# Performance work log

Measured on AMD Instinct MI355X. Metric: run time of the kernel, lower is better.

The kernel has to match this reference:

```python
import jax, jax.numpy as jnp
import numpy as np

B, T, D, VQ, L2, HID = 8, 2048, 768, 64, 12, 1024
K = 2 ** L2          # 4096 codebook entries
N_MID = 4            # condition_layer=6 -> 1 input + 4 middle + 1 output Linear, 5 BatchNorms
EPS_N = 1e-6
EPS_BN = 1e-5


def setup_inputs() -> dict:
    key = jax.random.key(0)
    ks = jax.random.split(key, 10)
    g = lambda i, shape, sc: jax.random.normal(ks[i], shape, jnp.float32) * sc
    return {
        "h_in": jax.random.normal(ks[0], (B, D, T), jnp.float32),
        "attn_mask": jax.random.randint(ks[1], (B, T), 0, 2, jnp.int32),
        "proj_w": g(2, (VQ, D), 0.02), "proj_b": jnp.zeros((VQ,), jnp.float32),
        "inv_w": g(3, (D, VQ), 0.02), "inv_b": jnp.zeros((D,), jnp.float32),
        "mlp_w_in": g(4, (HID, L2), 0.1), "mlp_b_in": jnp.zeros((HID,), jnp.float32),
        "mlp_w_mid": g(5, (N_MID, HID, HID), 0.03), "mlp_b_mid": jnp.zeros((N_MID, HID), jnp.float32),
        "mlp_w_out": g(6, (VQ, HID), 0.03), "mlp_b_out": jnp.zeros((VQ,), jnp.float32),
        "bn_gamma": jnp.ones((N_MID + 1, HID), jnp.float32),
        "bn_beta": jnp.zeros((N_MID + 1, HID), jnp.float32),
    }


def _bn(x, gamma, beta):
    # BatchNorm1d, training mode: batch mean / biased var over codebook rows
    m = x.mean(axis=0)
    v = x.var(axis=0)
    return (x - m) * jax.lax.rsqrt(v + EPS_BN) * gamma + beta


def _l2norm(x):
    return x / (jnp.linalg.norm(x, axis=-1, keepdims=True) + EPS_N)


def reference(h_in, attn_mask, proj_w, proj_b, inv_w, inv_b,
              mlp_w_in, mlp_b_in, mlp_w_mid, mlp_b_mid, mlp_w_out, mlp_b_out,
              bn_gamma, bn_beta):
    # --- codebook: binary vectors -> condition MLP (Linear+BN+ReLU x5, Linear) ---
    ints = jnp.arange(K)
    bits = ((ints[:, None] & (1 << jnp.arange(L2 - 1, -1, -1))) > 0).astype(jnp.float32)  # [K, L2]
    x = jax.nn.relu(_bn(bits @ mlp_w_in.T + mlp_b_in, bn_gamma[0], bn_beta[0]))
    for i in range(N_MID):
        x = jax.nn.relu(_bn(x @ mlp_w_mid[i].T + mlp_b_mid[i], bn_gamma[i + 1], bn_beta[i + 1]))
    embed = x @ mlp_w_out.T + mlp_b_out          # [K, VQ]
    embed = _l2norm(embed)                        # sphere=True

    # --- project hidden states: h_in [B,D,T] -> [B,T,VQ] ---
    h = jnp.einsum('bdt,vd->btv', h_in, proj_w) + proj_b
    h = _l2norm(h)

    # --- pairwise squared distances to codebook, argmax of -d (== softmax argmax) ---
    hf = h.reshape(-1, VQ)                                       # [B*T, VQ]
    d = (hf ** 2).sum(-1, keepdims=True) + (embed ** 2).sum(-1) - 2.0 * (hf @ embed.T)  # [B*T, K]
    code = jnp.argmax(-d, axis=-1)                               # [B*T]

    # --- masked gather/scatter quantization (eval path: hard codes) ---
    mask = (attn_mask == 1)                                      # [B, T]
    h_vq = embed[code].reshape(B, T, VQ) * mask[..., None].astype(h.dtype)
    quantized = jnp.einsum('btv,dv->btd', h_vq, inv_w) + inv_b   # proj_inv -> [B, T, D]
    vq_code = jnp.where(mask, code.reshape(B, T), 0)
    return quantized, vq_code
```

## Files before the change

kernel.cpp:

```cpp
#include <hip/hip_runtime.h>
#include <stddef.h>

#define BB   8
#define TT_  2048
#define DD   768
#define VQ_  64
#define L2C  12
#define HID_ 1024
#define KK   4096
#define NMID 4
#define NT   (BB*TT_)

typedef _Float16 h8v __attribute__((ext_vector_type(8)));
typedef float    f4v __attribute__((ext_vector_type(4)));

#define GL16(g, l) __builtin_amdgcn_global_load_lds( \
    (const __attribute__((address_space(1))) void*)(g), \
    (__attribute__((address_space(3))) void*)(l), 16, 0, 0)

__global__ __launch_bounds__(256) void k_mlp_in(const float* __restrict__ w_in,
                                                const float* __restrict__ b_in,
                                                float* __restrict__ X) {
    __shared__ float ws_[256 * 12];
    __shared__ float bs_[256];
    int tid = threadIdx.x;
    int h0  = blockIdx.x * 256;
    for (int i = tid; i < 256 * 12; i += 256) ws_[i] = w_in[h0 * 12 + i];
    bs_[tid] = b_in[h0 + tid];
    __syncthreads();
    float w[12];
#pragma unroll
    for (int l = 0; l < 12; l++) w[l] = ws_[tid * 12 + l];
    float bias = bs_[tid];
    int k0 = blockIdx.y * 16;
    for (int kk = 0; kk < 16; kk++) {
        int k = k0 + kk;
        float acc = bias;
#pragma unroll
        for (int l = 0; l < 12; l++)
            if ((k >> (11 - l)) & 1) acc += w[l];
        X[(size_t)k * HID_ + h0 + tid] = acc;
    }
}

__global__ __launch_bounds__(256) void k_bn_stats1(const float* __restrict__ Y,
                                                   float* __restrict__ part) {
    int b = blockIdx.x;
    int c = blockIdx.y * 256 + threadIdx.x;
    const float* src = Y + ((size_t)b << 6) * HID_ + c;
    float s = 0.f, q = 0.f;
    for (int r = 0; r < 64; r++) {
        float v = src[(size_t)r << 10];
        s += v; q += v * v;
    }
    part[((size_t)b << 10) + c] = s;
    part[65536 + ((size_t)b << 10) + c] = q;
}

__global__ __launch_bounds__(256) void k_bn_stats2(const float* __restrict__ part,
                                                   float* __restrict__ mv) {
    int c = blockIdx.x * 256 + threadIdx.x;
    float s = 0.f, q = 0.f;
    for (int b = 0; b < 64; b++) {
        s += part[((size_t)b << 10) + c];
        q += part[65536 + ((size_t)b << 10) + c];
    }
    float m = s * (1.f / KK);
    float v = q * (1.f / KK) - m * m;
    mv[c] = m; mv[HID_ + c] = v;
}

__global__ __launch_bounds__(256) void k_bn_apply_split(const float* __restrict__ Y,
                                                        const float* __restrict__ mv,
                                                        const float* __restrict__ gamma,
                                                        const float* __restrict__ beta,
                                                        _Float16* __restrict__ Xhi,
                                                        _Float16* __restrict__ Xlo) {
    int i = blockIdx.x * 256 + threadIdx.x;
    int c = (i << 2) & (HID_ - 1);
    float4 x = ((const float4*)Y)[i];
    float4 m = *(const float4*)(mv + c);
    float4 v = *(const float4*)(mv + HID_ + c);
    float4 g = *(const float4*)(gamma + c);
    float4 b = *(const float4*)(beta + c);
    float o[4];
    o[0] = fmaxf(0.f, (x.x - m.x) * (1.f / sqrtf(v.x + 1e-5f)) * g.x + b.x);
    o[1] = fmaxf(0.f, (x.y - m.y) * (1.f / sqrtf(v.y + 1e-5f)) * g.y + b.y);
    o[2] = fmaxf(0.f, (x.z - m.z) * (1.f / sqrtf(v.z + 1e-5f)) * g.z + b.z);
    o[3] = fmaxf(0.f, (x.w - m.w) * (1.f / sqrtf(v.w + 1e-5f)) * g.w + b.w);
    union { _Float16 h[4]; uint2 u; } uh, ul;
#pragma unroll
    for (int j = 0; j < 4; j++) {
        _Float16 h = (_Float16)o[j];
        uh.h[j] = h;
        ul.h[j] = (_Float16)(o[j] - (float)h);
    }
    *(uint2*)(Xhi + ((size_t)i << 2)) = uh.u;
    *(uint2*)(Xlo + ((size_t)i << 2)) = ul.u;
}

__global__ __launch_bounds__(256) void k_gemm_mfma3(const _Float16* __restrict__ Ahi,
                                                    const _Float16* __restrict__ Alo,
                                                    const _Float16* __restrict__ Whi,
                                                    const _Float16* __restrict__ Wlo,
                                                    const float* __restrict__ bias,
                                                    float* __restrict__ C) {
    __shared__ __attribute__((aligned(128))) char lds[4 * 32768];
    const int tid = threadIdx.x;
    const int wg = blockIdx.x;
    const int m0 = (wg & 31) << 7;
    const int n0 = (wg >> 5) << 7;
    const int wave = tid >> 6, lane = tid & 63;
    const int l15 = lane & 15, quad = lane >> 4;
    const int wm = (wave >> 1) << 6;
    const int wn = (wave & 1) << 6;

    const int rowA = (wave << 5) + (lane >> 2);
    const int colb = (lane & 3) << 4;
    const char* gA_h = (const char*)Ahi + ((size_t)(m0 + rowA) << 11) + colb;
    const char* gA_l = (const char*)Alo + ((size_t)(m0 + rowA) << 11) + colb;
    const char* gW_h = (const char*)Whi + ((size_t)(n0 + rowA) << 11) + colb;
    const char* gW_l = (const char*)Wlo + ((size_t)(n0 + rowA) << 11) + colb;
    const int dA = wave << 11;

    int offA[4], offW[4];
#pragma unroll
    for (int i = 0; i < 4; i++) offA[i] = ((wm + (i << 4) + l15) << 6) + (quad << 4);
#pragma unroll
    for (int j = 0; j < 4; j++) offW[j] = ((wn + (j << 4) + l15) << 6) + (quad << 4);

    f4v acc[4][4];
#pragma unroll
    for (int i = 0; i < 4; i++)
#pragma unroll
        for (int j = 0; j < 4; j++) acc[i][j] = (f4v){0.f, 0.f, 0.f, 0.f};

#define STG(bufi, tt) do { \
        char* b_ = lds + ((bufi) << 15); int o_ = (tt) << 6; \
        GL16(gA_h + o_,         b_ + dA); \
        GL16(gA_h + 32768 + o_, b_ + dA + 1024); \
        GL16(gA_l + o_,         b_ + 8192 + dA); \
        GL16(gA_l + 32768 + o_, b_ + 8192 + dA + 1024); \
        GL16(gW_h + o_,         b_ + 16384 + dA); \
        GL16(gW_h + 32768 + o_, b_ + 16384 + dA + 1024); \
        GL16(gW_l + o_,         b_ + 24576 + dA); \
        GL16(gW_l + 32768 + o_, b_ + 24576 + dA + 1024); \
    } while (0)

    STG(0, 0); STG(1, 1); STG(2, 2);
    for (int t = 0; t < 32; ++t) {
        if (t <= 29)      asm volatile("s_waitcnt vmcnt(16)" ::: "memory");
        else if (t == 30) asm volatile("s_waitcnt vmcnt(8)"  ::: "memory");
        else              asm volatile("s_waitcnt vmcnt(0)"  ::: "memory");
        __builtin_amdgcn_s_barrier();
        asm volatile("" ::: "memory");
        if (t + 3 < 32) STG((t + 3) & 3, t + 3);
        const char* b = lds + ((size_t)(t & 3) << 15);
        h8v ah[4], al[4];
#pragma unroll
        for (int i = 0; i < 4; i++) {
            ah[i] = *(const h8v*)(b + offA[i]);
            al[i] = *(const h8v*)(b + 8192 + offA[i]);
        }
        __builtin_amdgcn_s_setprio(1);
#pragma unroll
        for (int j = 0; j < 4; j++) {
            h8v bh = *(const h8v*)(b + 16384 + offW[j]);
            h8v bl = *(const h8v*)(b + 24576 + offW[j]);
#pragma unroll
            for (int i = 0; i < 4; i++) {
                acc[i][j] = __builtin_amdgcn_mfma_f32_16x16x32_f16(ah[i], bh, acc[i][j], 0, 0, 0);
                acc[i][j] = __builtin_amdgcn_mfma_f32_16x16x32_f16(ah[i], bl, acc[i][j], 0, 0, 0);
                acc[i][j] = __builtin_amdgcn_mfma_f32_16x16x32_f16(al[i], bh, acc[i][j], 0, 0, 0);
            }
        }
        __builtin_amdgcn_s_setprio(0);
        asm volatile("" ::: "memory");
    }
#undef STG

#pragma unroll
    for (int j = 0; j < 4; j++) {
        int col = n0 + wn + (j << 4) + l15;
        float bv = bias[col];
#pragma unroll
        for (int i = 0; i < 4; i++) {
            int row = m0 + wm + (i << 4) + (quad << 2);
#pragma unroll
            for (int r = 0; r < 4; r++)
                C[(size_t)(row + r) * HID_ + col] = acc[i][j][r] + bv;
        }
    }
}

__global__ __launch_bounds__(256) void k_gemm_mfma2(const _Float16* __restrict__ Ahi,
                                                    const _Float16* __restrict__ Alo,
                                                    const _Float16* __restrict__ Whi,
                                                    const _Float16* __restrict__ Wlo,
                                                    const float* __restrict__ bias,
                                                    float* __restrict__ C,
                                                    int M, int N, int Kd) {
    __shared__ __attribute__((aligned(128))) char lds[2][24576];
    const int tid = threadIdx.x;
    int wg = blockIdx.x;
    const int nwg = gridDim.x;
    wg = (wg & 7) * (nwg >> 3) + (wg >> 3);
    const int nx = M >> 7;
    const int m0 = (wg % nx) << 7;
    const int n0 = (wg / nx) << 6;
    const int wave = tid >> 6, lane = tid & 63;
    const int l15 = lane & 15, quad = lane >> 4;
    const int wm = (wave >> 1) << 6;
    const int wn = (wave & 1) << 5;

    const int pA0 = ((wave << 1) | 0) * 1024 + lane * 16;
    const int pA1 = ((wave << 1) | 1) * 1024 + lane * 16;
    const int pW  = wave * 1024 + lane * 16;
    const int qA0 = pA0 ^ (((pA0 >> 7) & 3) << 4);
    const int qA1 = pA1 ^ (((pA1 >> 7) & 3) << 4);
    const int qW  = pW  ^ (((pW  >> 7) & 3) << 4);
    const size_t krow = (size_t)Kd * 2;
    const char* gAh0 = (const char*)Ahi + (size_t)(m0 + (qA0 >> 6)) * krow + (qA0 & 63);
    const char* gAh1 = (const char*)Ahi + (size_t)(m0 + (qA1 >> 6)) * krow + (qA1 & 63);
    const char* gAl0 = (const char*)Alo + (size_t)(m0 + (qA0 >> 6)) * krow + (qA0 & 63);
    const char* gAl1 = (const char*)Alo + (size_t)(m0 + (qA1 >> 6)) * krow + (qA1 & 63);
    const char* gWh  = (const char*)Whi + (size_t)(n0 + (qW >> 6)) * krow + (qW & 63);
    const char* gWl  = (const char*)Wlo + (size_t)(n0 + (qW >> 6)) * krow + (qW & 63);
    const int dA0 = (wave << 1) * 1024;
    const int dA1 = dA0 + 1024;
    const int dW  = wave * 1024;

    int offA[4], offW[2];
#pragma unroll
    for (int i = 0; i < 4; i++) {
        int r = wm + (i << 4) + l15;
        offA[i] = r * 64 + ((quad ^ ((r >> 1) & 3)) << 4);
    }
#pragma unroll
    for (int j = 0; j < 2; j++) {
        int r = wn + (j << 4) + l15;
        offW[j] = r * 64 + ((quad ^ ((r >> 1) & 3)) << 4);
    }

    f4v acc[4][2];
#pragma unroll
    for (int i = 0; i < 4; i++)
#pragma unroll
        for (int j = 0; j < 2; j++) acc[i][j] = (f4v){0.f, 0.f, 0.f, 0.f};

#define STAGE(bufi, tt) do { \
        char* b_ = lds[bufi]; size_t o_ = (size_t)(tt) << 6; \
        GL16(gAh0 + o_, b_ + dA0); \
        GL16(gAh1 + o_, b_ + dA1); \
        GL16(gAl0 + o_, b_ + 8192 + dA0); \
        GL16(gAl1 + o_, b_ + 8192 + dA1); \
        GL16(gWh  + o_, b_ + 16384 + dW); \
        GL16(gWl  + o_, b_ + 20480 + dW); \
    } while (0)

    STAGE(0, 0);
    const int nt = Kd >> 5;
    for (int t = 0; t < nt; ++t) {
        const int cur = t & 1;
        if (t + 1 < nt) {
            STAGE(cur ^ 1, t + 1);
            asm volatile("s_waitcnt vmcnt(6)" ::: "memory");
        } else {
            asm volatile("s_waitcnt vmcnt(0)" ::: "memory");
        }
        __builtin_amdgcn_s_barrier();
        asm volatile("" ::: "memory");
        const char* b = lds[cur];
        h8v ah[4], al[4], bh[2], bl[2];
#pragma unroll
        for (int i = 0; i < 4; i++) {
            ah[i] = *(const h8v*)(b + offA[i]);
            al[i] = *(const h8v*)(b + 8192 + offA[i]);
        }
#pragma unroll
        for (int j = 0; j < 2; j++) {
            bh[j] = *(const h8v*)(b + 16384 + offW[j]);
            bl[j] = *(const h8v*)(b + 20480 + offW[j]);
        }
        __builtin_amdgcn_s_setprio(1);
#pragma unroll
        for (int i = 0; i < 4; i++)
#pragma unroll
            for (int j = 0; j < 2; j++) {
                acc[i][j] = __builtin_amdgcn_mfma_f32_16x16x32_f16(ah[i], bh[j], acc[i][j], 0, 0, 0);
                acc[i][j] = __builtin_amdgcn_mfma_f32_16x16x32_f16(ah[i], bl[j], acc[i][j], 0, 0, 0);
                acc[i][j] = __builtin_amdgcn_mfma_f32_16x16x32_f16(al[i], bh[j], acc[i][j], 0, 0, 0);
            }
        __builtin_amdgcn_s_setprio(0);
        asm volatile("" ::: "memory");
        __builtin_amdgcn_s_barrier();
    }
#undef STAGE

#pragma unroll
    for (int j = 0; j < 2; j++) {
        int col = n0 + wn + (j << 4) + l15;
        float bv = bias[col];
#pragma unroll
        for (int i = 0; i < 4; i++) {
            int row = m0 + wm + (i << 4) + (quad << 2);
#pragma unroll
            for (int r = 0; r < 4; r++)
                C[(size_t)(row + r) * N + col] = acc[i][j][r] + bv;
        }
    }
}

__global__ __launch_bounds__(256) void k_l2norm(float* __restrict__ E,
                                                float* __restrict__ eqh,
                                                _Float16* __restrict__ Ehi,
                                                _Float16* __restrict__ Elo) {
    int tid = threadIdx.x;
    int row = blockIdx.x * 4 + (tid >> 6);
    int v = tid & 63;
    size_t off = ((size_t)row << 6) + v;
    float x = E[off];
    float ss = x * x;
#pragma unroll
    for (int o = 32; o; o >>= 1) ss += __shfl_xor(ss, o, 64);
    float inv = 1.f / (sqrtf(ss) + 1e-6f);
    float xn = x * inv;
    E[off] = xn;
    _Float16 hh = (_Float16)xn;
    Ehi[off] = hh;
    Elo[off] = (_Float16)(xn - (float)hh);
    if (v == 0) eqh[row] = -0.5f * (ss * inv * inv);
}

__global__ __launch_bounds__(256) void k_wsplit(const float* __restrict__ pw,
                                                _Float16* __restrict__ pwhi,
                                                _Float16* __restrict__ pwlo) {
    int i = blockIdx.x * 256 + threadIdx.x;
    float4 w = ((const float4*)pw)[i];
    float wf[4] = {w.x, w.y, w.z, w.w};
    union { _Float16 h[4]; uint2 u; } uh, ul;
#pragma unroll
    for (int j = 0; j < 4; j++) {
        _Float16 h = (_Float16)wf[j];
        uh.h[j] = h;
        ul.h[j] = (_Float16)(wf[j] - (float)h);
    }
    *(uint2*)(pwhi + ((size_t)i << 2)) = uh.u;
    *(uint2*)(pwlo + ((size_t)i << 2)) = ul.u;
}

__global__ __launch_bounds__(256) void k_cvt_inv(const float* __restrict__ iw,
                                                 _Float16* __restrict__ iwh) {
    int i = blockIdx.x * 256 + threadIdx.x;
    float4 w = ((const float4*)iw)[i];
    union { _Float16 h[4]; uint2 u; } uh;
    uh.h[0] = (_Float16)w.x; uh.h[1] = (_Float16)w.y;
    uh.h[2] = (_Float16)w.z; uh.h[3] = (_Float16)w.w;
    *(uint2*)(iwh + ((size_t)i << 2)) = uh.u;
}

__global__ __launch_bounds__(256) void k_proj_mfma(const float* __restrict__ h_in,
                                                   const _Float16* __restrict__ pwhi,
                                                   const _Float16* __restrict__ pwlo,
                                                   float* __restrict__ Hpart) {
    __shared__ float shA[128 * 33];
    const int tid = threadIdx.x;
    const int t0 = blockIdx.x * 128;
    const int ks = blockIdx.y;
    const int b = t0 >> 11;
    const int tloc0 = t0 & (TT_ - 1);
    const int wave = tid >> 6, lane = tid & 63;
    const int l15 = lane & 15, quad = lane >> 4;

    const int dl = tid >> 3;
    const int tg = (tid & 7) << 4;

    f4v acc[2][4];
#pragma unroll
    for (int i = 0; i < 2; i++)
#pragma unroll
        for (int j = 0; j < 4; j++) acc[i][j] = (f4v){0.f, 0.f, 0.f, 0.f};

    for (int kk = 0; kk < 6; kk++) {
        int dd0 = ks * 192 + kk * 32;
        const float* src = h_in + ((size_t)(b * DD + dd0 + dl) << 11) + tloc0 + tg;
        float4 g0 = *(const float4*)(src);
        float4 g1 = *(const float4*)(src + 4);
        float4 g2 = *(const float4*)(src + 8);
        float4 g3 = *(const float4*)(src + 12);
        __syncthreads();
        float gv[16] = {g0.x, g0.y, g0.z, g0.w, g1.x, g1.y, g1.z, g1.w,
                        g2.x, g2.y, g2.z, g2.w, g3.x, g3.y, g3.z, g3.w};
#pragma unroll
        for (int i = 0; i < 16; i++) shA[(tg + i) * 33 + dl] = gv[i];
        __syncthreads();

        h8v ah[2], al[2];
#pragma unroll
        for (int mt = 0; mt < 2; mt++) {
            const float* ap = &shA[((wave << 5) + (mt << 4) + l15) * 33 + (quad << 3)];
            float4 a0 = *(const float4*)(ap);
            float4 a1 = *(const float4*)(ap + 4);
            float av[8] = {a0.x, a0.y, a0.z, a0.w, a1.x, a1.y, a1.z, a1.w};
#pragma unroll
            for (int j = 0; j < 8; j++) {
                _Float16 h = (_Float16)av[j];
                ah[mt][j] = h;
                al[mt][j] = (_Float16)(av[j] - (float)h);
            }
        }
#pragma unroll
        for (int nt = 0; nt < 4; nt++) {
            size_t wb = (size_t)((nt << 4) + l15) * DD + dd0 + (quad << 3);
            h8v bh = *(const h8v*)(pwhi + wb);
            h8v bl = *(const h8v*)(pwlo + wb);
#pragma unroll
            for (int mt = 0; mt < 2; mt++) {
                acc[mt][nt] = __builtin_amdgcn_mfma_f32_16x16x32_f16(ah[mt], bh, acc[mt][nt], 0, 0, 0);
                acc[mt][nt] = __builtin_amdgcn_mfma_f32_16x16x32_f16(ah[mt], bl, acc[mt][nt], 0, 0, 0);
                acc[mt][nt] = __builtin_amdgcn_mfma_f32_16x16x32_f16(al[mt], bh, acc[mt][nt], 0, 0, 0);
            }
        }
    }
    float* dst = Hpart + ((size_t)ks << 20);
#pragma unroll
    for (int mt = 0; mt < 2; mt++) {
#pragma unroll
        for (int r = 0; r < 4; r++) {
            int t = t0 + (wave << 5) + (mt << 4) + (quad << 2) + r;
#pragma unroll
            for (int nt = 0; nt < 4; nt++)
                dst[((size_t)t << 6) + (nt << 4) + l15] = acc[mt][nt][r];
        }
    }
}

__global__ __launch_bounds__(256) void k_hnorm(const float* __restrict__ Hpart,
                                               const float* __restrict__ pb,
                                               _Float16* __restrict__ Hhi,
                                               _Float16* __restrict__ Hlo) {
    __shared__ float ssp[4][64];
    int tid = threadIdx.x;
    int tt = tid & 63, vg = tid >> 6;
    int t = blockIdx.x * 64 + tt;
    size_t base = ((size_t)t << 6) + (vg << 4);
    float o[16];
#pragma unroll
    for (int u = 0; u < 4; u++) {
        float4 p0 = *(const float4*)(Hpart + (0u << 20) + base + (u << 2));
        float4 p1 = *(const float4*)(Hpart + (1u << 20) + base + (u << 2));
        float4 p2 = *(const float4*)(Hpart + (2u << 20) + base + (u << 2));
        float4 p3 = *(const float4*)(Hpart + (3u << 20) + base + (u << 2));
        o[u * 4 + 0] = p0.x + p1.x + p2.x + p3.x;
        o[u * 4 + 1] = p0.y + p1.y + p2.y + p3.y;
        o[u * 4 + 2] = p0.z + p1.z + p2.z + p3.z;
        o[u * 4 + 3] = p0.w + p1.w + p2.w + p3.w;
    }
    float sp = 0.f;
#pragma unroll
    for (int j = 0; j < 16; j++) {
        o[j] += pb[(vg << 4) + j];
        sp = fmaf(o[j], o[j], sp);
    }
    ssp[vg][tt] = sp;
    __syncthreads();
    float ss = ssp[0][tt] + ssp[1][tt] + ssp[2][tt] + ssp[3][tt];
    float inv = 1.f / (sqrtf(ss) + 1e-6f);
    union { _Float16 h[8]; uint4 u; } uh0, uh1, ul0, ul1;
#pragma unroll
    for (int j = 0; j < 16; j++) {
        float xn = o[j] * inv;
        _Float16 hh = (_Float16)xn;
        _Float16 ll = (_Float16)(xn - (float)hh);
        if (j < 8) { uh0.h[j] = hh; ul0.h[j] = ll; }
        else       { uh1.h[j - 8] = hh; ul1.h[j - 8] = ll; }
    }
    *(uint4*)(Hhi + base)     = uh0.u;
    *(uint4*)(Hhi + base + 8) = uh1.u;
    *(uint4*)(Hlo + base)     = ul0.u;
    *(uint4*)(Hlo + base + 8) = ul1.u;
}

__global__ __launch_bounds__(256) void k_argmax_mfma(const _Float16* __restrict__ Hhi,
                                                     const _Float16* __restrict__ Hlo,
                                                     const _Float16* __restrict__ Ehi,
                                                     const _Float16* __restrict__ Elo,
                                                     const float* __restrict__ eqh,
                                                     float* __restrict__ ps,
                                                     int* __restrict__ pi) {
    int tid = threadIdx.x;
    int wave = tid >> 6, lane = tid & 63;
    int l15 = lane & 15, quad = lane >> 4;
    int t0 = blockIdx.x * 256 + wave * 64;
    int kh = blockIdx.y;
    const int kbase = kh << 8;

    h8v hh0[4], hh1[4], hl0[4], hl1[4];
#pragma unroll
    for (int s = 0; s < 4; s++) {
        size_t hb = (size_t)(t0 + (s << 4) + l15) * 64 + (quad << 3);
        hh0[s] = *(const h8v*)(Hhi + hb);
        hh1[s] = *(const h8v*)(Hhi + hb + 32);
        hl0[s] = *(const h8v*)(Hlo + hb);
        hl1[s] = *(const h8v*)(Hlo + hb + 32);
    }
    float best[4] = {-1e30f, -1e30f, -1e30f, -1e30f};
    int   idx[4]  = {0, 0, 0, 0};

    size_t eb = (size_t)(kbase + l15) * 64 + (quad << 3);
    h8v eh0 = *(const h8v*)(Ehi + eb);
    h8v eh1 = *(const h8v*)(Ehi + eb + 32);
    h8v el0 = *(const h8v*)(Elo + eb);
    h8v el1 = *(const h8v*)(Elo + eb + 32);
    float4 q4 = *(const float4*)(eqh + kbase + (quad << 2));

    for (int it = 0; it < 16; it++) {
        h8v ce0 = eh0, ce1 = eh1, cl0 = el0, cl1 = el1;
        float4 cq = q4;
        int k0 = kbase + (it << 4);
        int kn = k0 + 16;
        if (kn > KK - 16) kn = KK - 16;
        size_t ebn = (size_t)(kn + l15) * 64 + (quad << 3);
        eh0 = *(const h8v*)(Ehi + ebn);
        eh1 = *(const h8v*)(Ehi + ebn + 32);
        el0 = *(const h8v*)(Elo + ebn);
        el1 = *(const h8v*)(Elo + ebn + 32);
        q4 = *(const float4*)(eqh + kn + (quad << 2));

        f4v acc[4];
#pragma unroll
        for (int s = 0; s < 4; s++) acc[s] = (f4v){0.f, 0.f, 0.f, 0.f};
#pragma unroll
        for (int s = 0; s < 4; s++) acc[s] = __builtin_amdgcn_mfma_f32_16x16x32_f16(ce0, hh0[s], acc[s], 0, 0, 0);
#pragma unroll
        for (int s = 0; s < 4; s++) acc[s] = __builtin_amdgcn_mfma_f32_16x16x32_f16(ce1, hh1[s], acc[s], 0, 0, 0);
#pragma unroll
        for (int s = 0; s < 4; s++) acc[s] = __builtin_amdgcn_mfma_f32_16x16x32_f16(cl0, hh0[s], acc[s], 0, 0, 0);
#pragma unroll
        for (int s = 0; s < 4; s++) acc[s] = __builtin_amdgcn_mfma_f32_16x16x32_f16(cl1, hh1[s], acc[s], 0, 0, 0);
#pragma unroll
        for (int s = 0; s < 4; s++) acc[s] = __builtin_amdgcn_mfma_f32_16x16x32_f16(ce0, hl0[s], acc[s], 0, 0, 0);
#pragma unroll
        for (int s = 0; s < 4; s++) acc[s] = __builtin_amdgcn_mfma_f32_16x16x32_f16(ce1, hl1[s], acc[s], 0, 0, 0);
        float qv[4] = {cq.x, cq.y, cq.z, cq.w};
#pragma unroll
        for (int r = 0; r < 4; r++) {
            int k = k0 + (quad << 2) + r;
#pragma unroll
            for (int s = 0; s < 4; s++) {
                float sc = acc[s][r] + qv[r];
                if (sc > best[s]) { best[s] = sc; idx[s] = k; }
            }
        }
    }
#pragma unroll
    for (int m = 16; m <= 32; m <<= 1) {
#pragma unroll
        for (int s = 0; s < 4; s++) {
            float ob = __shfl_xor(best[s], m, 64);
            int   oi = __shfl_xor(idx[s], m, 64);
            if (ob > best[s] || (ob == best[s] && oi < idx[s])) { best[s] = ob; idx[s] = oi; }
        }
    }
    if (quad == 0) {
#pragma unroll
        for (int s = 0; s < 4; s++) {
            int t = t0 + (s << 4) + l15;
            ps[(size_t)t * 16 + kh] = best[s];
            pi[(size_t)t * 16 + kh] = idx[s];
        }
    }
}

__global__ __launch_bounds__(256) void k_merge(const float* __restrict__ ps,
                                               const int* __restrict__ pi,
                                               const int* __restrict__ mask,
                                               const _Float16* __restrict__ Ehi,
                                               _Float16* __restrict__ G16,
                                               float* __restrict__ outc) {
    __shared__ int codes[256];
    __shared__ int ms[256];
    int tid = threadIdx.x;
    int base = blockIdx.x << 8;
    int t = base + tid;
    float best = ps[(size_t)t * 16];
    int bi = pi[(size_t)t * 16];
#pragma unroll
    for (int s = 1; s < 16; s++) {
        float v = ps[(size_t)t * 16 + s];
        if (v > best) { best = v; bi = pi[(size_t)t * 16 + s]; }
    }
    int m = mask[t];
    codes[tid] = bi;
    ms[tid] = m;
    outc[t] = m ? (float)bi : 0.0f;
    __syncthreads();
    for (int i = tid; i < 256 * 8; i += 256) {
        int r = i >> 3, u = i & 7;
        uint4 e = ms[r] ? ((const uint4*)(Ehi + ((size_t)codes[r] << 6)))[u]
                        : make_uint4(0u, 0u, 0u, 0u);
        ((uint4*)(G16 + ((size_t)(base + r) << 6)))[u] = e;
    }
}

__global__ __launch_bounds__(256) void k_gemm_out(const _Float16* __restrict__ G16,
                                                  const _Float16* __restrict__ iwh,
                                                  const float* __restrict__ bias,
                                                  float* __restrict__ C) {
    const int tid = threadIdx.x;
    const int t0 = blockIdx.x * 128, n0 = blockIdx.y * 64;
    const int wave = tid >> 6, lane = tid & 63;
    const int l15 = lane & 15, quad = lane >> 4;

    f4v acc[2][4];
#pragma unroll
    for (int i = 0; i < 2; i++)
#pragma unroll
        for (int j = 0; j < 4; j++) acc[i][j] = (f4v){0.f, 0.f, 0.f, 0.f};

#pragma unroll
    for (int ks = 0; ks < 2; ks++) {
        int kk = (ks << 5) + (quad << 3);
        h8v a[2], b[4];
#pragma unroll
        for (int mt = 0; mt < 2; mt++)
            a[mt] = *(const h8v*)(G16 + (size_t)(t0 + (wave << 5) + (mt << 4) + l15) * 64 + kk);
#pragma unroll
        for (int nt = 0; nt < 4; nt++)
            b[nt] = *(const h8v*)(iwh + (size_t)(n0 + (nt << 4) + l15) * 64 + kk);
#pragma unroll
        for (int mt = 0; mt < 2; mt++)
#pragma unroll
            for (int nt = 0; nt < 4; nt++)
                acc[mt][nt] = __builtin_amdgcn_mfma_f32_16x16x32_f16(a[mt], b[nt], acc[mt][nt], 0, 0, 0);
    }
#pragma unroll
    for (int nt = 0; nt < 4; nt++) {
        int col = n0 + (nt << 4) + l15;
        float bv = bias[col];
#pragma unroll
        for (int mt = 0; mt < 2; mt++) {
            int row = t0 + (wave << 5) + (mt << 4) + (quad << 2);
#pragma unroll
            for (int r = 0; r < 4; r++)
                C[(size_t)(row + r) * DD + col] = acc[mt][nt][r] + bv;
        }
    }
}

extern "C" void kernel_launch(void* const* d_in, const int* in_sizes, int n_in,
                              void* d_out, int out_size, void* d_ws, size_t ws_size,
                              hipStream_t stream) {
    const float* h_in   = (const float*)d_in[0];
    const int*   amask  = (const int*)d_in[1];
    const float* proj_w = (const float*)d_in[2];
    const float* proj_b = (const float*)d_in[3];
    const float* inv_w  = (const float*)d_in[4];
    const float* inv_b  = (const float*)d_in[5];
    const float* w_in   = (const float*)d_in[6];
    const float* b_in   = (const float*)d_in[7];
    const float* w_mid  = (const float*)d_in[8];
    const float* b_mid  = (const float*)d_in[9];
    const float* w_out  = (const float*)d_in[10];
    const float* b_out  = (const float*)d_in[11];
    const float* gamma  = (const float*)d_in[12];
    const float* beta   = (const float*)d_in[13];

    float*     Y    = (float*)d_ws;
    _Float16*  Xhi  = (_Float16*)(Y + (size_t)KK * HID_);
    _Float16*  Xlo  = Xhi + (size_t)KK * HID_;
    float*     mv   = (float*)(Xlo + (size_t)KK * HID_);
    float*     Emb  = mv + 2 * HID_;
    float*     eqh  = Emb + (size_t)KK * VQ_;
    float*     spart= eqh + KK;
    _Float16*  pwhi = (_Float16*)(spart + 2 * 65536);
    _Float16*  pwlo = pwhi + (size_t)VQ_ * DD;
    float*    Hpart = Y;
    _Float16* H16hi = Xhi;
    _Float16* H16lo = H16hi + (size_t)NT * VQ_;
    _Float16* E16hi = H16lo + (size_t)NT * VQ_;
    _Float16* E16lo = E16hi + (size_t)KK * VQ_;
    float*    ps    = (float*)(E16lo + (size_t)KK * VQ_);
    int*      pidx  = (int*)(ps + (size_t)NT * 16);
    _Float16* G16   = (_Float16*)(pidx + (size_t)NT * 16);
    _Float16* iwh   = G16 + (size_t)NT * VQ_;

    float* out_q = (float*)d_out;
    float* out_c = out_q + (size_t)NT * DD;

    _Float16* Wmh = (_Float16*)d_out;
    _Float16* Wml = Wmh + (size_t)HID_ * HID_;
    _Float16* Woh = Wml + (size_t)HID_ * HID_;
    _Float16* Wol = Woh + (size_t)VQ_ * HID_;

    k_mlp_in<<<dim3(HID_ / 256, KK / 16), 256, 0, stream>>>(w_in, b_in, Y);
    k_bn_stats1<<<dim3(64, 4), 256, 0, stream>>>(Y, spart);
    k_bn_stats2<<<4, 256, 0, stream>>>(spart, mv);
    k_bn_apply_split<<<KK * HID_ / 1024, 256, 0, stream>>>(Y, mv, gamma, beta, Xhi, Xlo);
    for (int i = 0; i < NMID; i++) {
        k_wsplit<<<HID_ * HID_ / 1024, 256, 0, stream>>>(
            w_mid + (size_t)i * HID_ * HID_, Wmh, Wml);
        k_gemm_mfma3<<<(KK / 128) * (HID_ / 128), 256, 0, stream>>>(
            Xhi, Xlo, Wmh, Wml, b_mid + (size_t)i * HID_, Y);
        k_bn_stats1<<<dim3(64, 4), 256, 0, stream>>>(Y, spart);
        k_bn_stats2<<<4, 256, 0, stream>>>(spart, mv);
        k_bn_apply_split<<<KK * HID_ / 1024, 256, 0, stream>>>(Y, mv,
            gamma + (size_t)(i + 1) * HID_, beta + (size_t)(i + 1) * HID_, Xhi, Xlo);
    }
    k_wsplit<<<VQ_ * HID_ / 1024, 256, 0, stream>>>(w_out, Woh, Wol);
    k_gemm_mfma2<<<(KK / 128) * (VQ_ / 64), 256, 0, stream>>>(
        Xhi, Xlo, Woh, Wol, b_out, Emb, KK, VQ_, HID_);
    k_l2norm<<<KK / 4, 256, 0, stream>>>(Emb, eqh, E16hi, E16lo);

    k_wsplit<<<VQ_ * DD / 1024, 256, 0, stream>>>(proj_w, pwhi, pwlo);
    k_cvt_inv<<<VQ_ * DD / 1024, 256, 0, stream>>>(inv_w, iwh);
    k_proj_mfma<<<dim3(NT / 128, 4), 256, 0, stream>>>(h_in, pwhi, pwlo, Hpart);
    k_hnorm<<<NT / 64, 256, 0, stream>>>(Hpart, proj_b, H16hi, H16lo);
    k_argmax_mfma<<<dim3(NT / 256, 16), 256, 0, stream>>>(
        H16hi, H16lo, E16hi, E16lo, eqh, ps, pidx);
    k_merge<<<NT / 256, 256, 0, stream>>>(ps, pidx, amask, E16hi, G16, out_c);
    k_gemm_out<<<dim3(NT / 128, DD / 64), 256, 0, stream>>>(G16, iwh, inv_b, out_q);
}
```

Measured before the change: 473.5 us.

## Stage codebook tiles through LDS in argmax and batch all weight splits

The argmax kernel now copies codebook hi/lo tiles and the norm terms into a swizzled 4-stage LDS ring buffer using async global-to-LDS loads with explicit vmcnt waits and barriers, shared by all four waves. Before, each wave read them from global memory into registers. It also raises MFMA issue priority and sets an occupancy hint. Separately, the six weight hi/lo split launches become one launch, which needs a larger scratch area in the output buffer for all four mid-layer weights. This saves launch overhead and duplicated codebook loads, at the cost of barrier synchronisation and more LDS per block.

```diff
diff --git a/kernel.cpp b/kernel.cpp
--- a/kernel.cpp
+++ b/kernel.cpp
@@ -332,11 +332,21 @@
     if (v == 0) eqh[row] = -0.5f * (ss * inv * inv);
 }
 
-__global__ __launch_bounds__(256) void k_wsplit(const float* __restrict__ pw,
-                                                _Float16* __restrict__ pwhi,
-                                                _Float16* __restrict__ pwlo) {
+__global__ __launch_bounds__(256) void k_wsplit_all(const float* __restrict__ w_mid,
+                                                    const float* __restrict__ w_out,
+                                                    const float* __restrict__ proj_w,
+                                                    _Float16* __restrict__ Wmh,
+                                                    _Float16* __restrict__ Wml,
+                                                    _Float16* __restrict__ Woh,
+                                                    _Float16* __restrict__ Wol,
+                                                    _Float16* __restrict__ pwhi,
+                                                    _Float16* __restrict__ pwlo) {
     int i = blockIdx.x * 256 + threadIdx.x;
-    float4 w = ((const float4*)pw)[i];
+    const float4* src; _Float16 *dh, *dl; int off;
+    if (i < 1048576)            { src = (const float4*)w_mid;  dh = Wmh;  dl = Wml;  off = i; }
+    else if (i < 1048576+16384) { src = (const float4*)w_out;  dh = Woh;  dl = Wol;  off = i - 1048576; }
+    else                        { src = (const float4*)proj_w; dh = pwhi; dl = pwlo; off = i - 1048576 - 16384; }
+    float4 w = src[off];
     float wf[4] = {w.x, w.y, w.z, w.w};
     union { _Float16 h[4]; uint2 u; } uh, ul;
 #pragma unroll
@@ -345,8 +355,8 @@
         uh.h[j] = h;
         ul.h[j] = (_Float16)(wf[j] - (float)h);
     }
-    *(uint2*)(pwhi + ((size_t)i << 2)) = uh.u;
-    *(uint2*)(pwlo + ((size_t)i << 2)) = ul.u;
+    *(uint2*)(dh + ((size_t)off << 2)) = uh.u;
+    *(uint2*)(dl + ((size_t)off << 2)) = ul.u;
 }
 
 __global__ __launch_bounds__(256) void k_cvt_inv(const float* __restrict__ iw,
@@ -481,13 +491,14 @@
     *(uint4*)(Hlo + base + 8) = ul1.u;
 }
 
-__global__ __launch_bounds__(256) void k_argmax_mfma(const _Float16* __restrict__ Hhi,
-                                                     const _Float16* __restrict__ Hlo,
-                                                     const _Float16* __restrict__ Ehi,
-                                                     const _Float16* __restrict__ Elo,
-                                                     const float* __restrict__ eqh,
-                                                     float* __restrict__ ps,
-                                                     int* __restrict__ pi) {
+__global__ __launch_bounds__(256, 4) void k_argmax_mfma(const _Float16* __restrict__ Hhi,
+                                                        const _Float16* __restrict__ Hlo,
+                                                        const _Float16* __restrict__ Ehi,
+                                                        const _Float16* __restrict__ Elo,
+                                                        const float* __restrict__ eqh,
+                                                        float* __restrict__ ps,
+                                                        int* __restrict__ pi) {
+    __shared__ __attribute__((aligned(128))) char elds[4 * 4096 + 1024];
     int tid = threadIdx.x;
     int wave = tid >> 6, lane = tid & 63;
     int l15 = lane & 15, quad = lane >> 4;
@@ -507,29 +518,40 @@
     float best[4] = {-1e30f, -1e30f, -1e30f, -1e30f};
     int   idx[4]  = {0, 0, 0, 0};
 
-    size_t eb = (size_t)(kbase + l15) * 64 + (quad << 3);
-    h8v eh0 = *(const h8v*)(Ehi + eb);
-    h8v eh1 = *(const h8v*)(Ehi + eb + 32);
-    h8v el0 = *(const h8v*)(Elo + eb);
-    h8v el1 = *(const h8v*)(Elo + eb + 32);
-    float4 q4 = *(const float4*)(eqh + kbase + (quad << 2));
-
-    for (int it = 0; it < 16; it++) {
-        h8v ce0 = eh0, ce1 = eh1, cl0 = el0, cl1 = el1;
-        float4 cq = q4;
-        int k0 = kbase + (it << 4);
-        int kn = k0 + 16;
-        if (kn > KK - 16) kn = KK - 16;
-        size_t ebn = (size_t)(kn + l15) * 64 + (quad << 3);
-        eh0 = *(const h8v*)(Ehi + ebn);
-        eh1 = *(const h8v*)(Ehi + ebn + 32);
-        el0 = *(const h8v*)(Elo + ebn);
-        el1 = *(const h8v*)(Elo + ebn + 32);
-        q4 = *(const float4*)(eqh + kn + (quad << 2));
+    const int p    = ((wave & 1) << 10) + lane * 16;
+    const int srow = p >> 7;
+    const int scol = (p & 127) ^ ((srow & 7) << 4);
+    const char* gsrc0 = (const char*)((wave < 2) ? Ehi : Elo)
+                      + (((size_t)kbase + srow) << 7) + scol;
+    const int dwave = wave << 10;
+#define ASTG(tt) GL16(gsrc0 + ((size_t)(tt) << 11), elds + (((tt) & 3) << 12) + dwave)
+
+    const int rswz = (l15 & 7) << 4;
+    const int o_e0 = l15 * 128 + ((quad << 4) ^ rswz);
+    const int o_e1 = l15 * 128 + ((64 + (quad << 4)) ^ rswz);
+
+    if (wave == 0) GL16((const char*)eqh + ((size_t)kbase << 2), elds + 16384);
+    ASTG(0); ASTG(1); ASTG(2);
+
+    for (int t = 0; t < 16; ++t) {
+        if (t <= 13)      asm volatile("s_waitcnt vmcnt(2)" ::: "memory");
+        else if (t == 14) asm volatile("s_waitcnt vmcnt(1)" ::: "memory");
+        else              asm volatile("s_waitcnt vmcnt(0)" ::: "memory");
+        __builtin_amdgcn_s_barrier();
+        asm volatile("" ::: "memory");
+        if (t + 3 < 16) ASTG(t + 3);
+        const char* b = elds + ((size_t)(t & 3) << 12);
+        h8v ce0 = *(const h8v*)(b + o_e0);
+        h8v ce1 = *(const h8v*)(b + o_e1);
+        h8v cl0 = *(const h8v*)(b + 2048 + o_e0);
+        h8v cl1 = *(const h8v*)(b + 2048 + o_e1);
+        float4 cq = *(const float4*)(elds + 16384 + (t << 6) + (quad << 4));
+        int k0 = kbase + (t << 4);
 
         f4v acc[4];
 #pragma unroll
         for (int s = 0; s < 4; s++) acc[s] = (f4v){0.f, 0.f, 0.f, 0.f};
+        __builtin_amdgcn_s_setprio(1);
 #pragma unroll
         for (int s = 0; s < 4; s++) acc[s] = __builtin_amdgcn_mfma_f32_16x16x32_f16(ce0, hh0[s], acc[s], 0, 0, 0);
 #pragma unroll
@@ -542,6 +564,7 @@
         for (int s = 0; s < 4; s++) acc[s] = __builtin_amdgcn_mfma_f32_16x16x32_f16(ce0, hl0[s], acc[s], 0, 0, 0);
 #pragma unroll
         for (int s = 0; s < 4; s++) acc[s] = __builtin_amdgcn_mfma_f32_16x16x32_f16(ce1, hl1[s], acc[s], 0, 0, 0);
+        __builtin_amdgcn_s_setprio(0);
         float qv[4] = {cq.x, cq.y, cq.z, cq.w};
 #pragma unroll
         for (int r = 0; r < 4; r++) {
@@ -552,7 +575,10 @@
                 if (sc > best[s]) { best[s] = sc; idx[s] = k; }
             }
         }
-    }
+        asm volatile("" ::: "memory");
+    }
+#undef ASTG
+
 #pragma unroll
     for (int m = 16; m <= 32; m <<= 1) {
 #pragma unroll
@@ -689,30 +715,30 @@
     float* out_c = out_q + (size_t)NT * DD;
 
     _Float16* Wmh = (_Float16*)d_out;
-    _Float16* Wml = Wmh + (size_t)HID_ * HID_;
-    _Float16* Woh = Wml + (size_t)HID_ * HID_;
+    _Float16* Wml = Wmh + (size_t)NMID * HID_ * HID_;
+    _Float16* Woh = Wml + (size_t)NMID * HID_ * HID_;
     _Float16* Wol = Woh + (size_t)VQ_ * HID_;
+
+    k_wsplit_all<<<4208, 256, 0, stream>>>(w_mid, w_out, proj_w,
+                                           Wmh, Wml, Woh, Wol, pwhi, pwlo);
 
     k_mlp_in<<<dim3(HID_ / 256, KK / 16), 256, 0, stream>>>(w_in, b_in, Y);
     k_bn_stats1<<<dim3(64, 4), 256, 0, stream>>>(Y, spart);
     k_bn_stats2<<<4, 256, 0, stream>>>(spart, mv);
     k_bn_apply_split<<<KK * HID_ / 1024, 256, 0, stream>>>(Y, mv, gamma, beta, Xhi, Xlo);
     for (int i = 0; i < NMID; i++) {
-        k_wsplit<<<HID_ * HID_ / 1024, 256, 0, stream>>>(
-            w_mid + (size_t)i * HID_ * HID_, Wmh, Wml);
         k_gemm_mfma3<<<(KK / 128) * (HID_ / 128), 256, 0, stream>>>(
-            Xhi, Xlo, Wmh, Wml, b_mid + (size_t)i * HID_, Y);
+            Xhi, Xlo, Wmh + (size_t)i * HID_ * HID_, Wml + (size_t)i * HID_ * HID_,
+            b_mid + (size_t)i * HID_, Y);
         k_bn_stats1<<<dim3(64, 4), 256, 0, stream>>>(Y, spart);
         k_bn_stats2<<<4, 256, 0, stream>>>(spart, mv);
         k_bn_apply_split<<<KK * HID_ / 1024, 256, 0, stream>>>(Y, mv,
             gamma + (size_t)(i + 1) * HID_, beta + (size_t)(i + 1) * HID_, Xhi, Xlo);
     }
-    k_wsplit<<<VQ_ * HID_ / 1024, 256, 0, stream>>>(w_out, Woh, Wol);
     k_gemm_mfma2<<<(KK / 128) * (VQ_ / 64), 256, 0, stream>>>(
         Xhi, Xlo, Woh, Wol, b_out, Emb, KK, VQ_, HID_);
     k_l2norm<<<KK / 4, 256, 0, stream>>>(Emb, eqh, E16hi, E16lo);
 
-    k_wsplit<<<VQ_ * DD / 1024, 256, 0, stream>>>(proj_w, pwhi, pwlo);
     k_cvt_inv<<<VQ_ * DD / 1024, 256, 0, stream>>>(inv_w, iwh);
     k_proj_mfma<<<dim3(NT / 128, 4), 256, 0, stream>>>(h_in, pwhi, pwlo, Hpart);
     k_hnorm<<<NT / 64, 256, 0, stream>>>(Hpart, proj_b, H16hi, H16lo);
```

New measurement: 453.3 us. 1.04x faster.
